# Performance work log

Measured on AMD Instinct MI355X. Metric: run time of the kernel, lower is better.

Reference implementation:

```python
import jax, jax.numpy as jnp
import numpy as np

B, E, S = 64, 256, 32        # batch, projection_size (=MHA embed dim), seq_l
H = 16                        # MHA heads
D_FINAL = 10                  # label space
K_CLASSES = D_FINAL * (D_FINAL - 1) // 2 + 1  # 46, header output dim
N_PATIENTS = 8
P_PAIRS = N_PATIENTS * (B // N_PATIENTS) ** 2  # 512 same-patient pairs (static)


def _pair_lookup(D):
    # class id of sorted label pair: (0,0)->0, then (a,b) a<b in lexicographic
    # order, matching torch.unique(rows of triu meshgrid) ordering.
    lut = np.zeros((D, D), np.int32)
    idx = 1
    for a in range(D):
        for b in range(a + 1, D):
            lut[a, b] = idx
            lut[b, a] = idx
            idx += 1
    return lut


def setup_inputs():
    ks = jax.random.split(jax.random.key(0), 10)
    s = 1.0 / np.sqrt(E)
    return {
        "features": jax.random.normal(ks[0], (B, E, S), jnp.float32),
        "labels0": jax.random.randint(ks[1], (B,), 0, D_FINAL, jnp.int32),
        "labels1": (jnp.arange(B, dtype=jnp.int32) // (B // N_PATIENTS)),
        "in_proj_w": jax.random.normal(ks[2], (3 * E, E), jnp.float32) * s,
        "in_proj_b": jax.random.normal(ks[3], (3 * E,), jnp.float32) * 0.01,
        "out_proj_w": jax.random.normal(ks[4], (E, E), jnp.float32) * s,
        "out_proj_b": jax.random.normal(ks[5], (E,), jnp.float32) * 0.01,
        "final_w": jax.random.normal(ks[6], (1, S), jnp.float32) * (1.0 / np.sqrt(S)),
        "final_b": jax.random.normal(ks[7], (1,), jnp.float32) * 0.01,
        "header_w": jax.random.normal(ks[8], (K_CLASSES, E), jnp.float32) * s,
        "header_b": jax.random.normal(ks[9], (K_CLASSES,), jnp.float32) * 0.01,
    }


def reference(features, labels0, labels1, in_proj_w, in_proj_b, out_proj_w,
              out_proj_b, final_w, final_b, header_w, header_b):
    # ---- pair selection: (i, j) with same patient id (labels1) ----
    mask = (labels1[:, None] == labels1[None, :]).reshape(-1)  # (B*B,)
    sel = jnp.nonzero(mask, size=P_PAIRS, fill_value=0)[0]      # row-major order
    valid = (jnp.arange(P_PAIRS) < mask.sum()).astype(jnp.float32)
    i_idx, j_idx = sel // B, sel % B                            # (P,), (P,)

    # ---- pair class labels: sorted (l_i, l_j), equal labels -> (0, 0) ----
    a, b = labels0[i_idx], labels0[j_idx]
    eq = a == b
    lo = jnp.where(eq, 0, jnp.minimum(a, b))
    hi = jnp.where(eq, 0, jnp.maximum(a, b))
    lut = jnp.asarray(_pair_lookup(D_FINAL))
    y = lut[lo, hi]                                             # (P,) class ids

    # ---- gather pair features; torch permutes to (2, P, seq_l, C) ----
    q_in = jnp.transpose(features[i_idx], (0, 2, 1))  # (P, S, E) query
    kv_in = jnp.transpose(features[j_idx], (0, 2, 1))  # (P, S, E) key/value

    # ---- MultiheadAttention (eval, dropout off); L = pair axis P, N = S ----
    Wq, Wk, Wv = jnp.split(in_proj_w, 3, axis=0)
    bq, bk, bv = jnp.split(in_proj_b, 3, axis=0)
    hd = E // H
    q = (q_in @ Wq.T + bq).reshape(P_PAIRS, S, H, hd)
    k = (kv_in @ Wk.T + bk).reshape(P_PAIRS, S, H, hd)
    v = (kv_in @ Wv.T + bv).reshape(P_PAIRS, S, H, hd)
    scores = jnp.einsum('lshd,mshd->shlm', q, k) / np.sqrt(hd)  # (S,H,P,P)
    attn = jax.nn.softmax(scores, axis=-1)
    o = jnp.einsum('shlm,mshd->lshd', attn, v).reshape(P_PAIRS, S, E)
    o = o @ out_proj_w.T + out_proj_b                           # (P, S, E)

    # ---- backbone.final: Linear over the seq axis (S -> 1), squeeze ----
    h = jnp.einsum('pse,s->pe', o, final_w[0]) + final_b[0]     # (P, E)
    logits = h @ header_w.T + header_b                          # (P, K)

    # ---- inverse-frequency class weights over selected pairs ----
    counts = jnp.zeros(K_CLASSES, jnp.float32).at[y].add(valid)
    w = jnp.where(counts > 0, 1.0 / jnp.maximum(counts, 1.0), 0.0)

    # ---- weighted cross-entropy (torch semantics: / sum of weights) ----
    nll = -jax.nn.log_softmax(logits, axis=-1)[jnp.arange(P_PAIRS), y]
    wy = w[y] * valid
    loss = jnp.sum(wy * nll) / jnp.sum(wy)
    return loss
```

## Files before the change

kernel.cpp:

```cpp
#include <hip/hip_runtime.h>
#include <math.h>

#define B_ 64
#define E_ 256
#define S_ 32
#define H_ 16
#define P_ 512
#define KC_ 46
#define QKV_N (B_*S_*E_)

#define WS_CM     0
#define WS_WK     256
#define WS_INVDEN 3328
#define WS_C      3392
#define WS_M      3584
#define WS_WB     16384
#define WS_XT     114688
#define WS_QKV    376832
#define WS_OPART  1949696

typedef short bf16x8 __attribute__((ext_vector_type(8)));
typedef float f32x4  __attribute__((ext_vector_type(4)));

__device__ __forceinline__ ushort f2bf(float f) {
  unsigned u = __float_as_uint(f);
  u = (u + 0x7FFFu + ((u >> 16) & 1u)) >> 16;
  return (ushort)u;
}

__global__ __launch_bounds__(256) void k_prep(
    const float* __restrict__ feat, const float* __restrict__ w,
    const int* __restrict__ labels0, const int* __restrict__ labels1,
    const float* __restrict__ wout, const float* __restrict__ bout,
    const float* __restrict__ fw, const float* __restrict__ fbi,
    const float* __restrict__ hw, const float* __restrict__ hb,
    float* __restrict__ ws, float* __restrict__ out) {
  __shared__ float sm[8448];
  const int bid = blockIdx.x, t = threadIdx.x;
  if (bid < 24) {
    const float4* src = (const float4*)w;
    ushort* dstW = (ushort*)(ws + WS_WB);
#pragma unroll
    for (int i = 0; i < 8; ++i) {
      int idx = bid*2048 + i*256 + t;
      float4 v = src[idx];
      ushort4 o;
      o.x = f2bf(v.x); o.y = f2bf(v.y); o.z = f2bf(v.z); o.w = f2bf(v.w);
      *(ushort4*)(dstW + (size_t)idx*4) = o;
    }
  } else if (bid < 88) {
    const int b = bid - 24;
    const float4* fb = (const float4*)(feat + (size_t)b*(E_*S_));
#pragma unroll
    for (int i = 0; i < 8; ++i) {
      int idx = i*256 + t; int e = idx >> 3, s4 = (idx & 7)*4;
      float4 v = fb[idx];
      sm[e*33 + s4+0] = v.x; sm[e*33 + s4+1] = v.y;
      sm[e*33 + s4+2] = v.z; sm[e*33 + s4+3] = v.w;
    }
    __syncthreads();
    const int s = t & 31, ec = (t >> 5) * 32;
    ushort* dstX = (ushort*)(ws + WS_XT) + (size_t)b*(S_*E_) + s*E_ + ec;
#pragma unroll
    for (int g = 0; g < 4; ++g) {
      ushort tmp[8];
#pragma unroll
      for (int u = 0; u < 8; ++u) tmp[u] = f2bf(sm[(ec + g*8 + u)*33 + s]);
      *(uint4*)(dstX + g*8) = *(uint4*)tmp;
    }
  } else if (bid == 88) {
    float* csh = sm;
    float* cls = sm + 64;
    float* wsh = sm + 112;
    float* den = sm + 160;
    float* Wk  = sm + 192;
    int* scan = (int*)(sm + 3200);
    int* l0   = (int*)(sm + 3456);
    int* l1   = (int*)(sm + 3520);
    int* seli = (int*)(sm + 3584);
    int* selj = (int*)(sm + 4096);
    if (t < 64) { l0[t] = labels0[t]; l1[t] = labels1[t]; csh[t] = 0.f; }
    if (t < KC_) cls[t] = 0.f;
    if (t == 0) den[0] = 0.f;
    for (int i = t; i < 2944; i += 256) Wk[i] = 0.f;
    __syncthreads();
    unsigned bits = 0; int c = 0;
    for (int u = 0; u < 16; ++u) {
      int idx = t*16 + u;
      if (l1[idx>>6] == l1[idx&63]) { bits |= 1u<<u; ++c; }
    }
    scan[t] = c; __syncthreads();
    for (int off = 1; off < 256; off <<= 1) {
      int v = (t >= off) ? scan[t-off] : 0;
      __syncthreads();
      scan[t] += v;
      __syncthreads();
    }
    const int total = scan[255];
    int rank = scan[t] - c;
    for (int p = t; p < P_; p += 256)
      if (p >= total) { seli[p] = 0; selj[p] = 0; }
    for (int u = 0; u < 16; ++u) {
      if (bits & (1u<<u)) {
        if (rank < P_) { int idx = t*16+u; seli[rank] = idx>>6; selj[rank] = idx&63; }
        ++rank;
      }
    }
    __syncthreads();
    int ii[2], yy[2]; float vv[2];
#pragma unroll
    for (int r = 0; r < 2; ++r) {
      int p = t + r*256;
      int i = seli[p], j = selj[p];
      atomicAdd(&csh[j], 1.0f);
      int la = l0[i], lb = l0[j];
      int y;
      if (la == lb) y = 0;
      else {
        int lo = la < lb ? la : lb, hi = la < lb ? lb : la;
        y = 1 + lo*9 - (lo*(lo-1))/2 + (hi-lo-1);
      }
      float v = (p < total) ? 1.f : 0.f;
      if (v > 0.f) atomicAdd(&cls[y], 1.f);
      ii[r] = i; yy[r] = y; vv[r] = v;
    }
    __syncthreads();
    if (t < KC_) {
      float cv = cls[t];
      wsh[t] = cv > 0.f ? 1.0f/cv : 0.f;
      if (cv > 0.f) atomicAdd(den, 1.0f);
    }
    __syncthreads();
#pragma unroll
    for (int r = 0; r < 2; ++r)
      if (vv[r] > 0.f) atomicAdd(&Wk[ii[r]*KC_ + yy[r]], wsh[yy[r]]);
    __syncthreads();
    if (t < 64) ws[WS_CM + t] = csh[t];
    for (int i = t; i < 2944; i += 256) ws[WS_WK + i] = Wk[i];
    if (t == 0) ws[WS_INVDEN] = 1.0f / den[0];
  } else if (bid < 135) {
    int k = bid - 89;
    float* hwsh = sm;
    float* redA = sm + 256;
    float* redB = sm + 512;
    hwsh[t] = hw[k*E_ + t];
    __syncthreads();
    float a0 = 0.f;
#pragma unroll 8
    for (int e = 0; e < E_; ++e) a0 = fmaf(hwsh[e], wout[e*E_ + t], a0);
    ws[WS_M + k*E_ + t] = a0;
    redA[t] = hwsh[t];
    redB[t] = hwsh[t]*bout[t];
    __syncthreads();
    for (int off = 128; off > 0; off >>= 1) {
      if (t < off) { redA[t] += redA[t+off]; redB[t] += redB[t+off]; }
      __syncthreads();
    }
    if (t == 0) {
      float sfw = 0.f;
      for (int s = 0; s < S_; ++s) sfw += fw[s];
      ws[WS_C + k] = fbi[0]*redA[0] + sfw*redB[0] + hb[k];
    }
  } else {
    if (t == 0) out[0] = 0.f;
  }
}

__global__ __launch_bounds__(256) void k_proj(
    const float* __restrict__ bias, float* __restrict__ ws) {
  const int bid = blockIdx.x, t = threadIdx.x;
  const int b = bid >> 3, w = t >> 6, L = t & 63;
  const int lane16 = L & 15, quad = L >> 4;
  const short* WB  = (const short*)(ws + WS_WB);
  const short* XTb = (const short*)(ws + WS_XT) + (size_t)b*(S_*E_);
#pragma unroll
  for (int i = 0; i < 3; ++i) {
    const int j = (bid & 7)*12 + w*3 + i;
    const int ot = j >> 1, st = j & 1;
    const int out0 = ot*16;
    const short* arow = WB  + (size_t)(out0 + lane16)*E_ + quad*8;
    const short* brow = XTb + (size_t)(st*16 + lane16)*E_ + quad*8;
    f32x4 acc = {0.f, 0.f, 0.f, 0.f};
#pragma unroll
    for (int k = 0; k < 8; ++k) {
      bf16x8 av = *(const bf16x8*)(arow + k*32);
      bf16x8 bv = *(const bf16x8*)(brow + k*32);
      acc = __builtin_amdgcn_mfma_f32_16x16x32_bf16(av, bv, acc, 0, 0, 0);
    }
    const int rgn = out0 >> 8;
    const int s = st*16 + lane16;
    const int e0 = (out0 & 255) + quad*4;
    float4 bb = *(const float4*)(bias + out0 + quad*4);
    float* dst = ws + WS_QKV + (size_t)rgn*QKV_N + (size_t)b*(S_*E_) + s*E_ + e0;
    *(float4*)dst = make_float4(acc[0]+bb.x, acc[1]+bb.y, acc[2]+bb.z, acc[3]+bb.w);
  }
}

__global__ __launch_bounds__(256) void k_attn(
    float* __restrict__ ws, const float* __restrict__ fw) {
  __shared__ float qT[16*68], kT[16*68], vs[64*20], sc[64*68], cm[64];
  const int s = blockIdx.x >> 4, h = blockIdx.x & 15;
  const int t = threadIdx.x;
  const int a = t >> 2, dq = t & 3;
  const float* qkv = ws + WS_QKV;
  {
    size_t off = (size_t)a*(S_*E_) + (size_t)s*E_ + h*16 + dq*4;
    float4 q4 = *(const float4*)(qkv + off);
    float4 k4 = *(const float4*)(qkv + QKV_N + off);
    float4 v4 = *(const float4*)(qkv + 2*(size_t)QKV_N + off);
    qT[(dq*4+0)*68 + a] = q4.x; qT[(dq*4+1)*68 + a] = q4.y;
    qT[(dq*4+2)*68 + a] = q4.z; qT[(dq*4+3)*68 + a] = q4.w;
    kT[(dq*4+0)*68 + a] = k4.x; kT[(dq*4+1)*68 + a] = k4.y;
    kT[(dq*4+2)*68 + a] = k4.z; kT[(dq*4+3)*68 + a] = k4.w;
    *(float4*)(vs + a*20 + dq*4) = v4;
  }
  if (t < 64) cm[t] = ws[WS_CM + t];
  __syncthreads();
  {
    const int ta = t & 15, tb = t >> 4;
    float sa[4][4];
#pragma unroll
    for (int r = 0; r < 4; ++r)
#pragma unroll
      for (int c = 0; c < 4; ++c) sa[r][c] = 0.f;
#pragma unroll
    for (int d = 0; d < 16; ++d) {
      float4 qv = *(float4*)(qT + d*68 + ta*4);
      float4 kv = *(float4*)(kT + d*68 + tb*4);
      float qr[4] = {qv.x,qv.y,qv.z,qv.w};
      float kc[4] = {kv.x,kv.y,kv.z,kv.w};
#pragma unroll
      for (int r = 0; r < 4; ++r)
#pragma unroll
        for (int c = 0; c < 4; ++c) sa[r][c] = fmaf(qr[r], kc[c], sa[r][c]);
    }
#pragma unroll
    for (int r = 0; r < 4; ++r)
      *(float4*)(sc + (ta*4+r)*68 + tb*4) =
          make_float4(sa[r][0]*0.25f, sa[r][1]*0.25f,
                      sa[r][2]*0.25f, sa[r][3]*0.25f);
  }
  __syncthreads();
  {
    float pv[16], cmv[16];
#pragma unroll
    for (int i4 = 0; i4 < 4; ++i4) {
      float4 v = *(float4*)(sc + a*68 + dq*16 + i4*4);
      pv[i4*4+0] = v.x; pv[i4*4+1] = v.y; pv[i4*4+2] = v.z; pv[i4*4+3] = v.w;
    }
#pragma unroll
    for (int i = 0; i < 16; ++i) cmv[i] = cm[dq*16 + i];
    float Mx = -1e30f;
#pragma unroll
    for (int i = 0; i < 16; ++i) if (cmv[i] > 0.f) Mx = fmaxf(Mx, pv[i]);
    Mx = fmaxf(Mx, __shfl_xor(Mx, 1));
    Mx = fmaxf(Mx, __shfl_xor(Mx, 2));
    float z = 0.f;
#pragma unroll
    for (int i = 0; i < 16; ++i) {
      float e = (cmv[i] > 0.f) ? cmv[i]*__expf(pv[i]-Mx) : 0.f;
      pv[i] = e; z += e;
    }
    z += __shfl_xor(z, 1);
    z += __shfl_xor(z, 2);
    float rz = 1.0f / z;
#pragma unroll
    for (int i4 = 0; i4 < 4; ++i4)
      *(float4*)(sc + a*68 + dq*16 + i4*4) =
          make_float4(pv[i4*4+0]*rz, pv[i4*4+1]*rz,
                      pv[i4*4+2]*rz, pv[i4*4+3]*rz);
  }
  __syncthreads();
  {
    const int g = t >> 6, l = t & 63;
    const int ar = g*16 + (l >> 2), d4 = (l & 3)*4;
    float o0 = 0.f, o1 = 0.f, o2 = 0.f, o3 = 0.f;
#pragma unroll 4
    for (int b4 = 0; b4 < 64; b4 += 4) {
      float4 p4 = *(float4*)(sc + ar*68 + b4);
      float4 va = *(float4*)(vs + (b4+0)*20 + d4);
      float4 vb = *(float4*)(vs + (b4+1)*20 + d4);
      float4 vc = *(float4*)(vs + (b4+2)*20 + d4);
      float4 vd = *(float4*)(vs + (b4+3)*20 + d4);
      o0 = fmaf(p4.x, va.x, fmaf(p4.y, vb.x, fmaf(p4.z, vc.x, fmaf(p4.w, vd.x, o0))));
      o1 = fmaf(p4.x, va.y, fmaf(p4.y, vb.y, fmaf(p4.z, vc.y, fmaf(p4.w, vd.y, o1))));
      o2 = fmaf(p4.x, va.z, fmaf(p4.y, vb.z, fmaf(p4.z, vc.z, fmaf(p4.w, vd.z, o2))));
      o3 = fmaf(p4.x, va.w, fmaf(p4.y, vb.w, fmaf(p4.z, vc.w, fmaf(p4.w, vd.w, o3))));
    }
    const float fwS = fw[s];
    float* dst = ws + WS_OPART + (size_t)s*(H_*B_*16) + h*(B_*16) + t*4;
    *(float4*)dst = make_float4(fwS*o0, fwS*o1, fwS*o2, fwS*o3);
  }
}

__global__ __launch_bounds__(256) void k_final(
    const float* __restrict__ ws, float* __restrict__ out) {
  const int aa = blockIdx.x, t = threadIdx.x;
  __shared__ float oh[256], lg[64];
  {
    const float* op = ws + WS_OPART + (t>>4)*(B_*16) + aa*16 + (t&15);
    float acc = 0.f;
#pragma unroll
    for (int s = 0; s < S_; ++s) acc += op[(size_t)s*(H_*B_*16)];
    oh[t] = acc;
  }
  __syncthreads();
  const int k = t >> 2, q = t & 3;
  if (k < KC_) {
    float lv = 0.f;
    const float4* M4 = (const float4*)(ws + WS_M + k*E_ + q*64);
    const float4* o4 = (const float4*)(oh + q*64);
#pragma unroll
    for (int j = 0; j < 16; ++j) {
      float4 m = M4[j], o = o4[j];
      lv = fmaf(m.x, o.x, lv); lv = fmaf(m.y, o.y, lv);
      lv = fmaf(m.z, o.z, lv); lv = fmaf(m.w, o.w, lv);
    }
    lv += __shfl_xor(lv, 1);
    lv += __shfl_xor(lv, 2);
    if (q == 0) lg[k] = lv + ws[WS_C + k];
  }
  __syncthreads();
  if (t < 64) {
    float x = (t < KC_) ? lg[t] : -1e30f;
    float Mx = x;
#pragma unroll
    for (int off = 1; off < 64; off <<= 1) Mx = fmaxf(Mx, __shfl_xor(Mx, off));
    float z = (t < KC_) ? __expf(x - Mx) : 0.f;
#pragma unroll
    for (int off = 1; off < 64; off <<= 1) z += __shfl_xor(z, off);
    float lse = Mx + __logf(z);
    float term = (t < KC_) ? ws[WS_WK + aa*KC_ + t] * (lse - x) : 0.f;
#pragma unroll
    for (int off = 1; off < 64; off <<= 1) term += __shfl_xor(term, off);
    if (t == 0) atomicAdd(out, term * ws[WS_INVDEN]);
  }
}

extern "C" void kernel_launch(void* const* d_in, const int* in_sizes, int n_in,
                              void* d_out, int out_size, void* d_ws, size_t ws_size,
                              hipStream_t stream) {
  const float* feat    = (const float*)d_in[0];
  const int*   labels0 = (const int*)d_in[1];
  const int*   labels1 = (const int*)d_in[2];
  const float* ipw     = (const float*)d_in[3];
  const float* ipb     = (const float*)d_in[4];
  const float* opw     = (const float*)d_in[5];
  const float* opb     = (const float*)d_in[6];
  const float* fw      = (const float*)d_in[7];
  const float* fbi     = (const float*)d_in[8];
  const float* hw      = (const float*)d_in[9];
  const float* hb      = (const float*)d_in[10];
  float* out = (float*)d_out;
  float* ws  = (float*)d_ws;

  k_prep<<<136, 256, 0, stream>>>(feat, ipw, labels0, labels1, opw, opb, fw,
                                  fbi, hw, hb, ws, out);
  k_proj<<<512, 256, 0, stream>>>(ipb, ws);
  k_attn<<<512, 256, 0, stream>>>(ws, fw);
  k_final<<<64, 256, 0, stream>>>(ws, out);
}
```

Baseline: 114.0 us.

## Fuse QKV projection into attention kernel and drop fp32 QKV round-trip

The separate projection kernel is removed. Each attention block (one seq position, one head) now computes its own Q, K and V slices with bf16 MFMA directly from a seq-major bf16 copy of the features, writing them into shared memory. The features are stored in a new layout so each block reads contiguous rows, and the 1/sqrt(hd) scale is folded into Q. This removes a kernel launch and the write and re-read of the large fp32 QKV buffer, at the cost of more MFMA and weight loads inside each attention block.

```diff
diff --git a/kernel.cpp b/kernel.cpp
--- a/kernel.cpp
+++ b/kernel.cpp
@@ -7,7 +7,6 @@
 #define H_ 16
 #define P_ 512
 #define KC_ 46
-#define QKV_N (B_*S_*E_)
 
 #define WS_CM     0
 #define WS_WK     256
@@ -15,8 +14,7 @@
 #define WS_C      3392
 #define WS_M      3584
 #define WS_WB     16384
-#define WS_XT     114688
-#define WS_QKV    376832
+#define WS_XF     114688
 #define WS_OPART  1949696
 
 typedef short bf16x8 __attribute__((ext_vector_type(8)));
@@ -59,13 +57,13 @@
       sm[e*33 + s4+2] = v.z; sm[e*33 + s4+3] = v.w;
     }
     __syncthreads();
-    const int s = t & 31, ec = (t >> 5) * 32;
-    ushort* dstX = (ushort*)(ws + WS_XT) + (size_t)b*(S_*E_) + s*E_ + ec;
+    const int s = t >> 3, eb = (t & 7) * 32;
+    ushort* dstX = (ushort*)(ws + WS_XF) + (size_t)s*(B_*E_) + (size_t)b*E_ + eb;
 #pragma unroll
     for (int g = 0; g < 4; ++g) {
       ushort tmp[8];
 #pragma unroll
-      for (int u = 0; u < 8; ++u) tmp[u] = f2bf(sm[(ec + g*8 + u)*33 + s]);
+      for (int u = 0; u < 8; ++u) tmp[u] = f2bf(sm[(eb + g*8 + u)*33 + s]);
       *(uint4*)(dstX + g*8) = *(uint4*)tmp;
     }
   } else if (bid == 88) {
@@ -166,53 +164,46 @@
   }
 }
 
-__global__ __launch_bounds__(256) void k_proj(
-    const float* __restrict__ bias, float* __restrict__ ws) {
-  const int bid = blockIdx.x, t = threadIdx.x;
-  const int b = bid >> 3, w = t >> 6, L = t & 63;
-  const int lane16 = L & 15, quad = L >> 4;
-  const short* WB  = (const short*)(ws + WS_WB);
-  const short* XTb = (const short*)(ws + WS_XT) + (size_t)b*(S_*E_);
-#pragma unroll
-  for (int i = 0; i < 3; ++i) {
-    const int j = (bid & 7)*12 + w*3 + i;
-    const int ot = j >> 1, st = j & 1;
-    const int out0 = ot*16;
-    const short* arow = WB  + (size_t)(out0 + lane16)*E_ + quad*8;
-    const short* brow = XTb + (size_t)(st*16 + lane16)*E_ + quad*8;
-    f32x4 acc = {0.f, 0.f, 0.f, 0.f};
-#pragma unroll
-    for (int k = 0; k < 8; ++k) {
-      bf16x8 av = *(const bf16x8*)(arow + k*32);
-      bf16x8 bv = *(const bf16x8*)(brow + k*32);
-      acc = __builtin_amdgcn_mfma_f32_16x16x32_bf16(av, bv, acc, 0, 0, 0);
-    }
-    const int rgn = out0 >> 8;
-    const int s = st*16 + lane16;
-    const int e0 = (out0 & 255) + quad*4;
-    float4 bb = *(const float4*)(bias + out0 + quad*4);
-    float* dst = ws + WS_QKV + (size_t)rgn*QKV_N + (size_t)b*(S_*E_) + s*E_ + e0;
-    *(float4*)dst = make_float4(acc[0]+bb.x, acc[1]+bb.y, acc[2]+bb.z, acc[3]+bb.w);
-  }
-}
-
 __global__ __launch_bounds__(256) void k_attn(
-    float* __restrict__ ws, const float* __restrict__ fw) {
+    const float* __restrict__ bias, const float* __restrict__ fw,
+    float* __restrict__ ws) {
   __shared__ float qT[16*68], kT[16*68], vs[64*20], sc[64*68], cm[64];
   const int s = blockIdx.x >> 4, h = blockIdx.x & 15;
   const int t = threadIdx.x;
+  const int w = t >> 6, L = t & 63, lane16 = L & 15, quad = L >> 4;
   const int a = t >> 2, dq = t & 3;
-  const float* qkv = ws + WS_QKV;
-  {
-    size_t off = (size_t)a*(S_*E_) + (size_t)s*E_ + h*16 + dq*4;
-    float4 q4 = *(const float4*)(qkv + off);
-    float4 k4 = *(const float4*)(qkv + QKV_N + off);
-    float4 v4 = *(const float4*)(qkv + 2*(size_t)QKV_N + off);
-    qT[(dq*4+0)*68 + a] = q4.x; qT[(dq*4+1)*68 + a] = q4.y;
-    qT[(dq*4+2)*68 + a] = q4.z; qT[(dq*4+3)*68 + a] = q4.w;
-    kT[(dq*4+0)*68 + a] = k4.x; kT[(dq*4+1)*68 + a] = k4.y;
-    kT[(dq*4+2)*68 + a] = k4.z; kT[(dq*4+3)*68 + a] = k4.w;
-    *(float4*)(vs + a*20 + dq*4) = v4;
+  {
+    const short* WB = (const short*)(ws + WS_WB);
+    const short* XF = (const short*)(ws + WS_XF);
+    const short* brow  = XF + (size_t)s*(B_*E_) + (size_t)(w*16 + lane16)*E_ + quad*8;
+    const short* arowQ = WB + (size_t)(      h*16 + lane16)*E_ + quad*8;
+    const short* arowK = WB + (size_t)(256 + h*16 + lane16)*E_ + quad*8;
+    const short* arowV = WB + (size_t)(512 + h*16 + lane16)*E_ + quad*8;
+    f32x4 accQ = {0.f,0.f,0.f,0.f}, accK = {0.f,0.f,0.f,0.f}, accV = {0.f,0.f,0.f,0.f};
+#pragma unroll
+    for (int k = 0; k < 8; ++k) {
+      bf16x8 bv = *(const bf16x8*)(brow  + k*32);
+      bf16x8 aq = *(const bf16x8*)(arowQ + k*32);
+      bf16x8 ak = *(const bf16x8*)(arowK + k*32);
+      bf16x8 av = *(const bf16x8*)(arowV + k*32);
+      accQ = __builtin_amdgcn_mfma_f32_16x16x32_bf16(aq, bv, accQ, 0, 0, 0);
+      accK = __builtin_amdgcn_mfma_f32_16x16x32_bf16(ak, bv, accK, 0, 0, 0);
+      accV = __builtin_amdgcn_mfma_f32_16x16x32_bf16(av, bv, accV, 0, 0, 0);
+    }
+    float4 bq = *(const float4*)(bias +        h*16 + quad*4);
+    float4 bk = *(const float4*)(bias + 256 + h*16 + quad*4);
+    float4 bv2 = *(const float4*)(bias + 512 + h*16 + quad*4);
+    const float bqa[4] = {bq.x,bq.y,bq.z,bq.w};
+    const float bka[4] = {bk.x,bk.y,bk.z,bk.w};
+    const float bva[4] = {bv2.x,bv2.y,bv2.z,bv2.w};
+    const int ag = w*16 + lane16;
+#pragma unroll
+    for (int r = 0; r < 4; ++r) {
+      int d = quad*4 + r;
+      qT[d*68 + ag] = (accQ[r] + bqa[r]) * 0.25f;
+      kT[d*68 + ag] =  accK[r] + bka[r];
+      vs[ag*20 + d] =  accV[r] + bva[r];
+    }
   }
   if (t < 64) cm[t] = ws[WS_CM + t];
   __syncthreads();
@@ -237,8 +228,7 @@
 #pragma unroll
     for (int r = 0; r < 4; ++r)
       *(float4*)(sc + (ta*4+r)*68 + tb*4) =
-          make_float4(sa[r][0]*0.25f, sa[r][1]*0.25f,
-                      sa[r][2]*0.25f, sa[r][3]*0.25f);
+          make_float4(sa[r][0], sa[r][1], sa[r][2], sa[r][3]);
   }
   __syncthreads();
   {
@@ -356,7 +346,6 @@
 
   k_prep<<<136, 256, 0, stream>>>(feat, ipw, labels0, labels1, opw, opb, fw,
                                   fbi, hw, hb, ws, out);
-  k_proj<<<512, 256, 0, stream>>>(ipb, ws);
-  k_attn<<<512, 256, 0, stream>>>(ws, fw);
+  k_attn<<<512, 256, 0, stream>>>(ipb, fw, ws);
   k_final<<<64, 256, 0, stream>>>(ws, out);
 }
```

After: 105.4 us. 1.08x faster.
